# Performance work log

Hardware: AMD Instinct MI355X
Metric: run time of the kernel (lower is better)

The kernel has to match this reference:

```python
import jax, jax.numpy as jnp
import numpy as np
from jax import lax

N_QUBITS = 8
DEPTH = 2
IN_DIM = 512
LN_EPS = 1e-5


def _ry_shared(state, w, theta_w):
    # RY(theta) on wire w, shared angle across the batch. state: [B, 2,...,2]
    ax = w + 1
    c = jnp.cos(theta_w / 2)
    s = jnp.sin(theta_w / 2)
    s0 = lax.index_in_dim(state, 0, axis=ax, keepdims=True)
    s1 = lax.index_in_dim(state, 1, axis=ax, keepdims=True)
    return jnp.concatenate([c * s0 - s * s1, s * s0 + c * s1], axis=ax)


def _cnot(state, cw, tw):
    # CNOT control=cw, target=tw. state: [B, 2,...,2]
    ax_c = cw + 1
    ax_t = tw + 1
    s0 = lax.index_in_dim(state, 0, axis=ax_c, keepdims=True)
    s1 = lax.index_in_dim(state, 1, axis=ax_c, keepdims=True)
    s1 = jnp.flip(s1, axis=ax_t)
    return jnp.concatenate([s0, s1], axis=ax_c)


def _circuit(angles, theta):
    # angles: [B, n]; theta: [n]. Batched statevector sim (RY/CNOT are real).
    B, n = angles.shape
    half = angles * 0.5
    c = jnp.cos(half)
    s = jnp.sin(half)
    # Initial RY layer on |0...0> is a product state: qubit i -> [cos, sin]
    state = jnp.ones((B,), dtype=angles.dtype)
    for i in range(n):
        amp = jnp.stack([c[:, i], s[:, i]], axis=-1)  # [B, 2]
        state = state[..., None] * amp.reshape((B,) + (1,) * i + (2,))
    # state: [B, 2, 2, ..., 2] (n qubit axes)
    for _ in range(DEPTH):
        for i in range(n):
            state = _cnot(state, i, (i + 1) % n)
        for i in range(n):
            state = _ry_shared(state, i, theta[i])
    # <Z_i> = P(bit_i=0) - P(bit_i=1)
    p = state * state
    zs = []
    for i in range(n):
        axes = tuple(a for a in range(1, n + 1) if a != i + 1)
        m = p.sum(axis=axes)  # [B, 2]
        zs.append(m[:, 0] - m[:, 1])
    return jnp.stack(zs, axis=-1)  # [B, n]


def setup_inputs() -> dict:
    key = jax.random.key(0)
    ks = jax.random.split(key, 6)
    B = 131072
    return {
        "E": jax.random.normal(ks[0], (B, IN_DIM), dtype=jnp.float32),
        "ln_gamma": jnp.ones((IN_DIM,), dtype=jnp.float32),
        "ln_beta": jnp.zeros((IN_DIM,), dtype=jnp.float32),
        "W_pre": jax.random.normal(ks[1], (N_QUBITS, IN_DIM), dtype=jnp.float32) * (1.0 / np.sqrt(IN_DIM)),
        "b_pre": jax.random.normal(ks[2], (N_QUBITS,), dtype=jnp.float32) * 0.02,
        "theta": jax.random.normal(ks[3], (N_QUBITS,), dtype=jnp.float32) * 0.1,
        "W_post": jax.random.normal(ks[4], (1, N_QUBITS), dtype=jnp.float32) * (1.0 / np.sqrt(N_QUBITS)),
        "b_post": jax.random.normal(ks[5], (1,), dtype=jnp.float32) * 0.02,
    }


def reference(E, ln_gamma, ln_beta, W_pre, b_pre, theta, W_post, b_post):
    # pre: LayerNorm + Linear(in_dim -> n_qubits)
    mu = E.mean(axis=-1, keepdims=True)
    var = ((E - mu) ** 2).mean(axis=-1, keepdims=True)
    x = (E - mu) * lax.rsqrt(var + LN_EPS) * ln_gamma + ln_beta
    angles = x @ W_pre.T + b_pre  # [B, n_qubits]
    Z = _circuit(angles, theta)  # [B, n_qubits]
    logit_known = (Z @ W_post.T + b_post)[:, 0]  # squeeze(-1)
    return logit_known
```

## Files before the change

kernel.cpp:

```cpp
#include <hip/hip_runtime.h>

#define BLOCK 256

typedef float v2f __attribute__((ext_vector_type(2)));

__device__ __forceinline__ float rfl(float x) {
  return __uint_as_float(__builtin_amdgcn_readfirstlane(__float_as_uint(x)));
}
__device__ __forceinline__ v2f mk2(float x, float y) { v2f r; r.x = x; r.y = y; return r; }
__device__ __forceinline__ v2f sp2(float x) { v2f r; r.x = x; r.y = x; return r; }
__device__ __forceinline__ v2f pkfma(v2f a, v2f b, v2f c) {
  return __builtin_elementwise_fma(a, b, c);
}
__device__ __forceinline__ v2f swap2(v2f v) { return __builtin_shufflevector(v, v, 1, 0); }

template<int CTRL>
__device__ __forceinline__ float dppmov(float x) {
  return __int_as_float(__builtin_amdgcn_update_dpp(
      0, __float_as_int(x), CTRL, 0xf, 0xf, true));
}
__device__ __forceinline__ float dx1(float x) { return dppmov<0xB1>(x); }
__device__ __forceinline__ float dx2(float x) { return dppmov<0x4E>(x); }
__device__ __forceinline__ float dswap13(float x) { return dppmov<0x6C>(x); }
__device__ __forceinline__ float dx4(float x) {
  return dppmov<0x1B>(dppmov<0x141>(x));
}
__device__ __forceinline__ float dx8(float x) { return dppmov<0x128>(x); }
__device__ __forceinline__ float sx16(float x) { return __shfl_xor(x, 16, 64); }
__device__ __forceinline__ float sx32(float x) { return __shfl_xor(x, 32, 64); }

__device__ __forceinline__ float wave_allsum(float x) {
  x += dx1(x); x += dx2(x); x += dx4(x); x += dx8(x);
  x += sx16(x); x += sx32(x);
  return x;
}


__global__ __launch_bounds__(BLOCK, 4) void qsco_kernel(
    const float* __restrict__ E,
    const float* __restrict__ ln_gamma,
    const float* __restrict__ ln_beta,
    const float* __restrict__ Wpre,
    const float* __restrict__ bpre,
    const float* __restrict__ theta,
    const float* __restrict__ Wpost,
    const float* __restrict__ bpost,
    float* __restrict__ out,
    int nrows)
{
  __shared__ float Wg[8][512];

  const int tid  = threadIdx.x;
  const int lane = tid & 63;

#pragma unroll
  for (int t = 0; t < 4; ++t) {
    const int e4 = (t * BLOCK + tid) << 2;
    const int j = e4 >> 9, k = e4 & 511;
    const float4 w = *(const float4*)(Wpre + j * 512 + k);
    const float4 g = *(const float4*)(ln_gamma + k);
    float4 r;
    r.x = w.x * g.x; r.y = w.y * g.y; r.z = w.z * g.z; r.w = w.w * g.w;
    *(float4*)(&Wg[j][k]) = r;
  }
  __syncthreads();

  const int k0 = lane << 3;
  const float4 gamA = *(const float4*)(ln_gamma + k0);
  const float4 gamB = *(const float4*)(ln_gamma + k0 + 4);
  const float4 betA = *(const float4*)(ln_beta + k0);
  const float4 betB = *(const float4*)(ln_beta + k0 + 4);
  float G[8], K[8];
#pragma unroll
  for (int j = 0; j < 8; ++j) {
    const float4 wA = *(const float4*)(Wpre + j * 512 + k0);
    const float4 wB = *(const float4*)(Wpre + j * 512 + k0 + 4);
    const float gs = wA.x*gamA.x + wA.y*gamA.y + wA.z*gamA.z + wA.w*gamA.w
                   + wB.x*gamB.x + wB.y*gamB.y + wB.z*gamB.z + wB.w*gamB.w;
    const float ks = wA.x*betA.x + wA.y*betA.y + wA.z*betA.z + wA.w*betA.w
                   + wB.x*betB.x + wB.y*betB.y + wB.z*betB.z + wB.w*betB.w;
    G[j] = rfl(wave_allsum(gs));
    K[j] = rfl(wave_allsum(ks) + bpre[j]);
  }

  float cT[8], sT[8];
#pragma unroll
  for (int q = 0; q < 8; ++q) {
    const float h = 0.5f * theta[q];
    cT[q] = rfl(__cosf(h));
    sT[q] = rfl(__sinf(h));
  }
  const float ss6 = (lane & 1) ? sT[6] : -sT[6];
  const float ss7 = (lane & 2) ? sT[7] : -sT[7];

  float al[8];
#pragma unroll
  for (int q = 0; q < 8; ++q) al[q] = rfl(Wpost[q]);
  const float lsign = ((lane & 1) ? -al[6] : al[6]) + ((lane & 2) ? -al[7] : al[7]);
  const float bp = rfl(bpost[0]);

  const int wave = blockIdx.x * (BLOCK / 64) + (tid >> 6);
  const int row  = wave * 16 + (lane >> 2);
  const int sub  = lane & 3;
  const float* Erow = E + (size_t)(row < nrows ? row : 0) * 512 + (sub << 2);

  v2f f2[10];
#pragma unroll
  for (int t = 0; t < 10; ++t) f2[t] = sp2(0.f);
#pragma unroll 4
  for (int i = 0; i < 32; ++i) {
    const float4 ev = *(const float4*)(Erow + (i << 4));
    const v2f eA = mk2(ev.x, ev.y), eB = mk2(ev.z, ev.w);
    const int kk = (sub << 2) + (i << 4);
    f2[0] += eA + eB;
    f2[1] = pkfma(eA, eA, pkfma(eB, eB, f2[1]));
#pragma unroll
    for (int j = 0; j < 8; ++j) {
      const float4 w = *(const float4*)(&Wg[j][kk]);
      f2[2 + j] = pkfma(eA, mk2(w.x, w.y), pkfma(eB, mk2(w.z, w.w), f2[2 + j]));
    }
  }
  float f[10];
#pragma unroll
  for (int t = 0; t < 10; ++t) f[t] = f2[t].x + f2[t].y;
#pragma unroll
  for (int t = 0; t < 10; ++t) f[t] += dx1(f[t]);
#pragma unroll
  for (int t = 0; t < 10; ++t) f[t] += dx2(f[t]);

  const float mu   = f[0] * (1.0f / 512.0f);
  const float var  = f[1] * (1.0f / 512.0f) - mu * mu;
  const float rstd = rsqrtf(var + 1e-5f);

  float ca[8], sa[8];
#pragma unroll
  for (int j = 0; j < 8; ++j) {
    const float ang = rstd * (f[2 + j] - mu * G[j]) + K[j];
    const float h = 0.5f * ang;
    ca[j] = __cosf(h);
    sa[j] = __sinf(h);
  }

  v2f a2[32];
  {
    const float base = ((lane & 1) ? sa[6] : ca[6]) * ((lane & 2) ? sa[7] : ca[7]);
    a2[0] = mk2(ca[5] * base, sa[5] * base);
#pragma unroll
    for (int b = 0; b < 5; ++b) {
      const int m = 1 << b;
      const v2f cb = sp2(ca[b]), sb = sp2(sa[b]);
#pragma unroll
      for (int k = 0; k < 16; ++k) {
        if (k < m) {
          a2[k + m] = a2[k] * sb;
          a2[k]     = a2[k] * cb;
        }
      }
    }
  }

  const v2f cT2_0 = sp2(cT[0]), sT2_0 = sp2(sT[0]), nT2_0 = sp2(-sT[0]);
  const v2f cT2_1 = sp2(cT[1]), sT2_1 = sp2(sT[1]), nT2_1 = sp2(-sT[1]);
  const v2f cT2_2 = sp2(cT[2]), sT2_2 = sp2(sT[2]), nT2_2 = sp2(-sT[2]);
  const v2f cT2_3 = sp2(cT[3]), sT2_3 = sp2(sT[3]), nT2_3 = sp2(-sT[3]);
  const v2f cT2_4 = sp2(cT[4]), sT2_4 = sp2(sT[4]), nT2_4 = sp2(-sT[4]);
  const v2f cT2_5 = sp2(cT[5]);
  const v2f sm5   = mk2(-sT[5], sT[5]);
  const v2f cT2_6 = sp2(cT[6]), ss6v = sp2(ss6);
  const v2f cT2_7 = sp2(cT[7]), ss7v = sp2(ss7);

#define RY_REG(CC, SS, NN, M) { \
    _Pragma("unroll") \
    for (int k = 0; k < 32; ++k) if (!(k & (M))) { \
      const v2f x = a2[k], y = a2[k | (M)]; \
      a2[k]       = pkfma(NN, y, CC * x); \
      a2[k | (M)] = pkfma(SS, x, CC * y); \
    } }

#pragma unroll
  for (int d = 0; d < 2; ++d) {
#pragma unroll
    for (int k = 0; k < 32; ++k) if ((k & 1) && !(k & 2)) {
      const v2f t_ = a2[k]; a2[k] = a2[k ^ 2]; a2[k ^ 2] = t_;
    }
#pragma unroll
    for (int k = 0; k < 32; ++k) if ((k & 2) && !(k & 4)) {
      const v2f t_ = a2[k]; a2[k] = a2[k ^ 4]; a2[k ^ 4] = t_;
    }
#pragma unroll
    for (int k = 0; k < 32; ++k) if ((k & 4) && !(k & 8)) {
      const v2f t_ = a2[k]; a2[k] = a2[k ^ 8]; a2[k ^ 8] = t_;
    }
#pragma unroll
    for (int k = 0; k < 32; ++k) if ((k & 8) && !(k & 16)) {
      const v2f t_ = a2[k]; a2[k] = a2[k ^ 16]; a2[k ^ 16] = t_;
    }
#pragma unroll
    for (int k = 16; k < 32; ++k) a2[k] = swap2(a2[k]);
#pragma unroll
    for (int k = 0; k < 32; ++k) a2[k].y = dx1(a2[k].y);
#pragma unroll
    for (int k = 0; k < 32; ++k) {
      a2[k].x = dswap13(a2[k].x);
      a2[k].y = dswap13(a2[k].y);
    }
    {
      const bool c = (lane & 2) != 0;
#pragma unroll
      for (int m = 0; m < 16; ++m) {
        const v2f x = a2[2 * m], y = a2[2 * m + 1];
        a2[2 * m].x     = c ? y.x : x.x;
        a2[2 * m].y     = c ? y.y : x.y;
        a2[2 * m + 1].x = c ? x.x : y.x;
        a2[2 * m + 1].y = c ? x.y : y.y;
      }
    }
    RY_REG(cT2_0, sT2_0, nT2_0, 1)
    RY_REG(cT2_1, sT2_1, nT2_1, 2)
    RY_REG(cT2_2, sT2_2, nT2_2, 4)
    RY_REG(cT2_3, sT2_3, nT2_3, 8)
    RY_REG(cT2_4, sT2_4, nT2_4, 16)
#pragma unroll
    for (int k = 0; k < 32; ++k) {
      const v2f t_ = swap2(a2[k]);
      a2[k] = pkfma(sm5, t_, cT2_5 * a2[k]);
    }
#pragma unroll
    for (int k = 0; k < 32; ++k) {
      const v2f p = mk2(dx1(a2[k].x), dx1(a2[k].y));
      a2[k] = pkfma(ss6v, p, cT2_6 * a2[k]);
    }
#pragma unroll
    for (int k = 0; k < 32; ++k) {
      const v2f p = mk2(dx2(a2[k].x), dx2(a2[k].y));
      a2[k] = pkfma(ss7v, p, cT2_7 * a2[k]);
    }
  }
#undef RY_REG

#pragma unroll
  for (int k = 0; k < 32; ++k) a2[k] = a2[k] * a2[k];
  v2f zr2[5];
#pragma unroll
  for (int b = 0; b < 5; ++b) {
    const int n = 16 >> b;
    v2f zb = sp2(0.f);
#pragma unroll
    for (int m = 0; m < 16; ++m) {
      if (m < n) {
        const v2f p = a2[2 * m], q = a2[2 * m + 1];
        zb   += (p - q);
        a2[m] = p + q;
      }
    }
    zr2[b] = zb;
  }
  const float z5  = a2[0].x - a2[0].y;
  const float tot = a2[0].x + a2[0].y;
  float vL = lsign * tot + al[5] * z5;
#pragma unroll
  for (int b = 0; b < 5; ++b) vL += al[b] * (zr2[b].x + zr2[b].y);
  vL += dx1(vL);
  vL += dx2(vL);
  if (sub == 0 && row < nrows) out[row] = vL + bp;
}

extern "C" void kernel_launch(void* const* d_in, const int* in_sizes, int n_in,
                              void* d_out, int out_size, void* d_ws, size_t ws_size,
                              hipStream_t stream) {
  const float* E        = (const float*)d_in[0];
  const float* ln_gamma = (const float*)d_in[1];
  const float* ln_beta  = (const float*)d_in[2];
  const float* Wpre     = (const float*)d_in[3];
  const float* bpre     = (const float*)d_in[4];
  const float* theta    = (const float*)d_in[5];
  const float* Wpost    = (const float*)d_in[6];
  const float* bpost    = (const float*)d_in[7];
  float* out = (float*)d_out;

  const int nrows = in_sizes[0] / 512;
  const int rows_per_block = (BLOCK / 64) * 16;
  const int grid = (nrows + rows_per_block - 1) / rows_per_block;
  qsco_kernel<<<grid, BLOCK, 0, stream>>>(E, ln_gamma, ln_beta, Wpre, bpre,
                                          theta, Wpost, bpost, out, nrows);
}
```

Measured before the change: 392.4 us.

## Split fused kernel into LayerNorm-projection and circuit kernels via workspace

Splits the single fused kernel into two launches. The first computes LayerNorm plus the 8-way projection and writes half-angles to a workspace buffer, with each wave handling two 16-row batches. The second reads those angles and runs the statevector circuit simulation. The aim is to stop the memory-bound streaming phase and the register-heavy compute phase from limiting each other's occupancy, at the cost of an extra launch and a round trip through global memory for the angles. The fused path is kept as a fallback when no workspace is available.

```diff
diff --git a/kernel.cpp b/kernel.cpp
--- a/kernel.cpp
+++ b/kernel.cpp
@@ -36,7 +36,293 @@
 }
 
 
-__global__ __launch_bounds__(BLOCK, 4) void qsco_kernel(
+__global__ __launch_bounds__(BLOCK, 4) void qsco_angles(
+    const float* __restrict__ E,
+    const float* __restrict__ ln_gamma,
+    const float* __restrict__ ln_beta,
+    const float* __restrict__ Wpre,
+    const float* __restrict__ bpre,
+    float* __restrict__ hang,
+    int nrows)
+{
+  __shared__ float Wg[8][512];
+
+  const int tid  = threadIdx.x;
+  const int lane = tid & 63;
+
+#pragma unroll
+  for (int t = 0; t < 4; ++t) {
+    const int e4 = (t * BLOCK + tid) << 2;
+    const int j = e4 >> 9, k = e4 & 511;
+    const float4 w = *(const float4*)(Wpre + j * 512 + k);
+    const float4 g = *(const float4*)(ln_gamma + k);
+    float4 r;
+    r.x = w.x * g.x; r.y = w.y * g.y; r.z = w.z * g.z; r.w = w.w * g.w;
+    *(float4*)(&Wg[j][k]) = r;
+  }
+  __syncthreads();
+
+  const int wave = blockIdx.x * (BLOCK / 64) + (tid >> 6);
+  if (wave * 32 >= nrows) return;
+
+  const int k0 = lane << 3;
+  const float4 gamA = *(const float4*)(ln_gamma + k0);
+  const float4 gamB = *(const float4*)(ln_gamma + k0 + 4);
+  const float4 betA = *(const float4*)(ln_beta + k0);
+  const float4 betB = *(const float4*)(ln_beta + k0 + 4);
+  float G[8], K[8];
+#pragma unroll
+  for (int j = 0; j < 8; ++j) {
+    const float4 wA = *(const float4*)(Wpre + j * 512 + k0);
+    const float4 wB = *(const float4*)(Wpre + j * 512 + k0 + 4);
+    const float gs = wA.x*gamA.x + wA.y*gamA.y + wA.z*gamA.z + wA.w*gamA.w
+                   + wB.x*gamB.x + wB.y*gamB.y + wB.z*gamB.z + wB.w*gamB.w;
+    const float ks = wA.x*betA.x + wA.y*betA.y + wA.z*betA.z + wA.w*betA.w
+                   + wB.x*betB.x + wB.y*betB.y + wB.z*betB.z + wB.w*betB.w;
+    G[j] = rfl(wave_allsum(gs));
+    K[j] = rfl(wave_allsum(ks) + bpre[j]);
+  }
+
+  const int sub = lane & 3;
+
+#define DOT_CHUNK(CUR, NXT, C, PREF) \
+  { if (PREF) { _Pragma("unroll") \
+      for (int i = 0; i < 8; ++i) \
+        NXT[i] = *(const float4*)(Erow + ((((C) + 1) * 8 + i) << 4)); } \
+    _Pragma("unroll") \
+    for (int i = 0; i < 8; ++i) { \
+      const float4 ev = CUR[i]; \
+      const v2f eA = mk2(ev.x, ev.y), eB = mk2(ev.z, ev.w); \
+      const int kk = (sub << 2) + (((C) * 8 + i) << 4); \
+      f2[0] += eA + eB; \
+      f2[1] = pkfma(eA, eA, pkfma(eB, eB, f2[1])); \
+      _Pragma("unroll") \
+      for (int j = 0; j < 8; ++j) { \
+        const float4 w = *(const float4*)(&Wg[j][kk]); \
+        f2[2 + j] = pkfma(eA, mk2(w.x, w.y), pkfma(eB, mk2(w.z, w.w), f2[2 + j])); \
+      } } }
+
+#pragma unroll
+  for (int bb = 0; bb < 2; ++bb) {
+    const int batch = wave * 2 + bb;
+    if (batch * 16 >= nrows) break;
+    const int row = batch * 16 + (lane >> 2);
+    const int rowc = row < nrows ? row : nrows - 1;
+    const float* Erow = E + (size_t)rowc * 512 + (sub << 2);
+
+    v2f f2[10];
+#pragma unroll
+    for (int t = 0; t < 10; ++t) f2[t] = sp2(0.f);
+
+    float4 b0[8], b1[8];
+#pragma unroll
+    for (int i = 0; i < 8; ++i) b0[i] = *(const float4*)(Erow + (i << 4));
+    DOT_CHUNK(b0, b1, 0, true)
+    DOT_CHUNK(b1, b0, 1, true)
+    DOT_CHUNK(b0, b1, 2, true)
+    DOT_CHUNK(b1, b0, 3, false)
+
+    float f[10];
+#pragma unroll
+    for (int t = 0; t < 10; ++t) f[t] = f2[t].x + f2[t].y;
+#pragma unroll
+    for (int t = 0; t < 10; ++t) f[t] += dx1(f[t]);
+#pragma unroll
+    for (int t = 0; t < 10; ++t) f[t] += dx2(f[t]);
+
+    const float mu   = f[0] * (1.0f / 512.0f);
+    const float var  = f[1] * (1.0f / 512.0f) - mu * mu;
+    const float rstd = rsqrtf(var + 1e-5f);
+
+    float h[8];
+#pragma unroll
+    for (int j = 0; j < 8; ++j)
+      h[j] = 0.5f * (rstd * (f[2 + j] - mu * G[j]) + K[j]);
+
+    if (row < nrows) {
+      if (sub == 0) {
+        float4 s; s.x = h[0]; s.y = h[1]; s.z = h[2]; s.w = h[3];
+        *(float4*)(hang + (size_t)row * 8) = s;
+      } else if (sub == 1) {
+        float4 s; s.x = h[4]; s.y = h[5]; s.z = h[6]; s.w = h[7];
+        *(float4*)(hang + (size_t)row * 8 + 4) = s;
+      }
+    }
+  }
+#undef DOT_CHUNK
+}
+
+
+__global__ __launch_bounds__(BLOCK, 4) void qsco_circuit(
+    const float* __restrict__ hang,
+    const float* __restrict__ theta,
+    const float* __restrict__ Wpost,
+    const float* __restrict__ bpost,
+    float* __restrict__ out,
+    int nrows)
+{
+  const int tid  = threadIdx.x;
+  const int lane = tid & 63;
+  const int wave = blockIdx.x * (BLOCK / 64) + (tid >> 6);
+  if (wave * 16 >= nrows) return;
+  const int row = wave * 16 + (lane >> 2);
+  const int sub = lane & 3;
+
+  float cT[8], sT[8];
+#pragma unroll
+  for (int q = 0; q < 8; ++q) {
+    const float h = 0.5f * theta[q];
+    cT[q] = rfl(__cosf(h));
+    sT[q] = rfl(__sinf(h));
+  }
+  const float ss6 = (lane & 1) ? sT[6] : -sT[6];
+  const float ss7 = (lane & 2) ? sT[7] : -sT[7];
+
+  float al[8];
+#pragma unroll
+  for (int q = 0; q < 8; ++q) al[q] = rfl(Wpost[q]);
+  const float lsign = ((lane & 1) ? -al[6] : al[6]) + ((lane & 2) ? -al[7] : al[7]);
+  const float bp = rfl(bpost[0]);
+
+  const int rowc = row < nrows ? row : nrows - 1;
+  const float4 h0 = *(const float4*)(hang + (size_t)rowc * 8);
+  const float4 h1 = *(const float4*)(hang + (size_t)rowc * 8 + 4);
+  float ca[8], sa[8];
+  ca[0] = __cosf(h0.x); sa[0] = __sinf(h0.x);
+  ca[1] = __cosf(h0.y); sa[1] = __sinf(h0.y);
+  ca[2] = __cosf(h0.z); sa[2] = __sinf(h0.z);
+  ca[3] = __cosf(h0.w); sa[3] = __sinf(h0.w);
+  ca[4] = __cosf(h1.x); sa[4] = __sinf(h1.x);
+  ca[5] = __cosf(h1.y); sa[5] = __sinf(h1.y);
+  ca[6] = __cosf(h1.z); sa[6] = __sinf(h1.z);
+  ca[7] = __cosf(h1.w); sa[7] = __sinf(h1.w);
+
+  v2f a2[32];
+  {
+    const float base = ((lane & 1) ? sa[6] : ca[6]) * ((lane & 2) ? sa[7] : ca[7]);
+    a2[0] = mk2(ca[5] * base, sa[5] * base);
+#pragma unroll
+    for (int b = 0; b < 5; ++b) {
+      const int m = 1 << b;
+      const v2f cb = sp2(ca[b]), sb = sp2(sa[b]);
+#pragma unroll
+      for (int k = 0; k < 16; ++k) {
+        if (k < m) {
+          a2[k + m] = a2[k] * sb;
+          a2[k]     = a2[k] * cb;
+        }
+      }
+    }
+  }
+
+  const v2f cT2_0 = sp2(cT[0]), sT2_0 = sp2(sT[0]), nT2_0 = sp2(-sT[0]);
+  const v2f cT2_1 = sp2(cT[1]), sT2_1 = sp2(sT[1]), nT2_1 = sp2(-sT[1]);
+  const v2f cT2_2 = sp2(cT[2]), sT2_2 = sp2(sT[2]), nT2_2 = sp2(-sT[2]);
+  const v2f cT2_3 = sp2(cT[3]), sT2_3 = sp2(sT[3]), nT2_3 = sp2(-sT[3]);
+  const v2f cT2_4 = sp2(cT[4]), sT2_4 = sp2(sT[4]), nT2_4 = sp2(-sT[4]);
+  const v2f cT2_5 = sp2(cT[5]);
+  const v2f sm5   = mk2(-sT[5], sT[5]);
+  const v2f cT2_6 = sp2(cT[6]), ss6v = sp2(ss6);
+  const v2f cT2_7 = sp2(cT[7]), ss7v = sp2(ss7);
+
+#define RY_REG(CC, SS, NN, M) { \
+    _Pragma("unroll") \
+    for (int k = 0; k < 32; ++k) if (!(k & (M))) { \
+      const v2f x = a2[k], y = a2[k | (M)]; \
+      a2[k]       = pkfma(NN, y, CC * x); \
+      a2[k | (M)] = pkfma(SS, x, CC * y); \
+    } }
+
+#pragma unroll
+  for (int d = 0; d < 2; ++d) {
+#pragma unroll
+    for (int k = 0; k < 32; ++k) if ((k & 1) && !(k & 2)) {
+      const v2f t_ = a2[k]; a2[k] = a2[k ^ 2]; a2[k ^ 2] = t_;
+    }
+#pragma unroll
+    for (int k = 0; k < 32; ++k) if ((k & 2) && !(k & 4)) {
+      const v2f t_ = a2[k]; a2[k] = a2[k ^ 4]; a2[k ^ 4] = t_;
+    }
+#pragma unroll
+    for (int k = 0; k < 32; ++k) if ((k & 4) && !(k & 8)) {
+      const v2f t_ = a2[k]; a2[k] = a2[k ^ 8]; a2[k ^ 8] = t_;
+    }
+#pragma unroll
+    for (int k = 0; k < 32; ++k) if ((k & 8) && !(k & 16)) {
+      const v2f t_ = a2[k]; a2[k] = a2[k ^ 16]; a2[k ^ 16] = t_;
+    }
+#pragma unroll
+    for (int k = 16; k < 32; ++k) a2[k] = swap2(a2[k]);
+#pragma unroll
+    for (int k = 0; k < 32; ++k) a2[k].y = dx1(a2[k].y);
+#pragma unroll
+    for (int k = 0; k < 32; ++k) {
+      a2[k].x = dswap13(a2[k].x);
+      a2[k].y = dswap13(a2[k].y);
+    }
+    {
+      const bool c = (lane & 2) != 0;
+#pragma unroll
+      for (int m = 0; m < 16; ++m) {
+        const v2f x = a2[2 * m], y = a2[2 * m + 1];
+        a2[2 * m].x     = c ? y.x : x.x;
+        a2[2 * m].y     = c ? y.y : x.y;
+        a2[2 * m + 1].x = c ? x.x : y.x;
+        a2[2 * m + 1].y = c ? x.y : y.y;
+      }
+    }
+    RY_REG(cT2_0, sT2_0, nT2_0, 1)
+    RY_REG(cT2_1, sT2_1, nT2_1, 2)
+    RY_REG(cT2_2, sT2_2, nT2_2, 4)
+    RY_REG(cT2_3, sT2_3, nT2_3, 8)
+    RY_REG(cT2_4, sT2_4, nT2_4, 16)
+#pragma unroll
+    for (int k = 0; k < 32; ++k) {
+      const v2f t_ = swap2(a2[k]);
+      a2[k] = pkfma(sm5, t_, cT2_5 * a2[k]);
+    }
+#pragma unroll
+    for (int k = 0; k < 32; ++k) {
+      const v2f p = mk2(dx1(a2[k].x), dx1(a2[k].y));
+      a2[k] = pkfma(ss6v, p, cT2_6 * a2[k]);
+    }
+#pragma unroll
+    for (int k = 0; k < 32; ++k) {
+      const v2f p = mk2(dx2(a2[k].x), dx2(a2[k].y));
+      a2[k] = pkfma(ss7v, p, cT2_7 * a2[k]);
+    }
+  }
+#undef RY_REG
+
+#pragma unroll
+  for (int k = 0; k < 32; ++k) a2[k] = a2[k] * a2[k];
+  v2f zr2[5];
+#pragma unroll
+  for (int b = 0; b < 5; ++b) {
+    const int n = 16 >> b;
+    v2f zb = sp2(0.f);
+#pragma unroll
+    for (int m = 0; m < 16; ++m) {
+      if (m < n) {
+        const v2f p = a2[2 * m], q = a2[2 * m + 1];
+        zb   += (p - q);
+        a2[m] = p + q;
+      }
+    }
+    zr2[b] = zb;
+  }
+  const float z5  = a2[0].x - a2[0].y;
+  const float tot = a2[0].x + a2[0].y;
+  float vL = lsign * tot + al[5] * z5;
+#pragma unroll
+  for (int b = 0; b < 5; ++b) vL += al[b] * (zr2[b].x + zr2[b].y);
+  vL += dx1(vL);
+  vL += dx2(vL);
+  if (sub == 0 && row < nrows) out[row] = vL + bp;
+}
+
+
+__global__ __launch_bounds__(BLOCK, 4) void qsco_fused(
     const float* __restrict__ E,
     const float* __restrict__ ln_gamma,
     const float* __restrict__ ln_beta,
@@ -49,10 +335,8 @@
     int nrows)
 {
   __shared__ float Wg[8][512];
-
   const int tid  = threadIdx.x;
   const int lane = tid & 63;
-
 #pragma unroll
   for (int t = 0; t < 4; ++t) {
     const int e4 = (t * BLOCK + tid) << 2;
@@ -279,8 +563,21 @@
   float* out = (float*)d_out;
 
   const int nrows = in_sizes[0] / 512;
-  const int rows_per_block = (BLOCK / 64) * 16;
-  const int grid = (nrows + rows_per_block - 1) / rows_per_block;
-  qsco_kernel<<<grid, BLOCK, 0, stream>>>(E, ln_gamma, ln_beta, Wpre, bpre,
-                                          theta, Wpost, bpost, out, nrows);
-}
+  const size_t need = (size_t)nrows * 8 * sizeof(float);
+
+  if (d_ws != nullptr && ws_size >= need) {
+    const int batches = (nrows + 15) / 16;
+    const int wavesA  = (batches + 1) / 2;
+    const int blocksA = (wavesA + 3) / 4;
+    const int blocksB = (batches + 3) / 4;
+    float* hang = (float*)d_ws;
+    qsco_angles<<<blocksA, BLOCK, 0, stream>>>(E, ln_gamma, ln_beta, Wpre, bpre,
+                                               hang, nrows);
+    qsco_circuit<<<blocksB, BLOCK, 0, stream>>>(hang, theta, Wpost, bpost, out, nrows);
+  } else {
+    const int rows_per_block = (BLOCK / 64) * 16;
+    const int grid = (nrows + rows_per_block - 1) / rows_per_block;
+    qsco_fused<<<grid, BLOCK, 0, stream>>>(E, ln_gamma, ln_beta, Wpre, bpre,
+                                           theta, Wpost, bpost, out, nrows);
+  }
+}
```

After: 404.1 us. 1.03x slower.
